# Optimization experiments

Measured on AMD Instinct MI355X. Metric: run time of the kernel, lower is better.

Reference implementation:

```python
import jax, jax.numpy as jnp
import numpy as np
import math

B, T, D_MODEL, N_HEADS = 4, 2048, 1024, 16
HEAD_DIM = D_MODEL // N_HEADS


def setup_inputs() -> dict:
    key = jax.random.key(0)
    k1, k2, k3 = jax.random.split(key, 3)
    x = jax.random.normal(k1, (B, T, D_MODEL), dtype=jnp.float32)
    # torch Linear weight layout: [out_features, in_features]
    w_qkv = jax.random.normal(k2, (3 * D_MODEL, D_MODEL), dtype=jnp.float32) * (1.0 / math.sqrt(D_MODEL))
    w_out = jax.random.normal(k3, (D_MODEL, D_MODEL), dtype=jnp.float32) * (1.0 / math.sqrt(D_MODEL))
    return {"x": x, "w_qkv": w_qkv, "w_out": w_out}


def reference(x, w_qkv, w_out):
    b, t, c = x.shape
    h, d = N_HEADS, HEAD_DIM
    # qkv projection: (B,T,3C) -> (3,B,H,T,D)
    qkv = jnp.einsum('btc,fc->btf', x, w_qkv)
    qkv = qkv.reshape(b, t, 3, h, d).transpose(2, 0, 3, 1, 4)
    q, k, v = qkv[0], qkv[1], qkv[2]
    scale = 1.0 / math.sqrt(d)
    # full O(T^2) attention scores, causal masked
    scores = jnp.einsum('bhqd,bhkd->bhqk', q, k) * scale
    causal = jnp.tril(jnp.ones((t, t), dtype=bool))
    scores = jnp.where(causal[None, None, :, :], scores, jnp.float32(-jnp.inf))
    attn = jax.nn.softmax(scores, axis=-1)
    out = jnp.einsum('bhqk,bhkd->bhqd', attn, v)  # (B,H,T,D)
    out = out.transpose(0, 2, 1, 3).reshape(b, t, c)
    out = jnp.einsum('btc,oc->bto', out, w_out)
    return out
```

## Files before the change

kernel.cpp:

```cpp
#include <hip/hip_runtime.h>
#include <hip/hip_bf16.h>

#define T_SEQ 2048
#define BATCH 4
#define NH    16
#define DM    1024
#define HD    64

typedef __attribute__((ext_vector_type(4))) float  f32x4;
typedef __attribute__((ext_vector_type(8))) short  s16x8;
typedef __attribute__((ext_vector_type(4))) short  s16x4;
typedef __attribute__((ext_vector_type(4))) unsigned short u16x4;

__device__ __forceinline__ unsigned short f2b(float f) {
  union { float f; unsigned u; } v; v.f = f;
  unsigned u = v.u;
  unsigned r = 0x7fffu + ((u >> 16) & 1u);
  u += r;
  return (unsigned short)(u >> 16);
}

__device__ __forceinline__ f32x4 mfma16(s16x8 a, s16x8 b, f32x4 c) {
  return __builtin_amdgcn_mfma_f32_16x16x32_bf16(a, b, c, 0, 0, 0);
}

__global__ void cvt_all(const float* __restrict__ x, const float* __restrict__ wq,
                        const float* __restrict__ wo,
                        unsigned short* __restrict__ xb, unsigned short* __restrict__ wqb,
                        unsigned short* __restrict__ wob) {
  const int N4X = (BATCH * T_SEQ * DM) / 4;
  const int N4Q = (3 * DM * DM) / 4;
  const int N4O = (DM * DM) / 4;
  const int N4QSCALED = (DM * DM) / 4;
  int i = blockIdx.x * blockDim.x + threadIdx.x;
  int stride = gridDim.x * blockDim.x;
  for (int j = i; j < N4X + N4Q + N4O; j += stride) {
    const float* src; unsigned short* dst; int k; float scale = 1.f;
    if (j < N4X) { src = x; dst = xb; k = j; }
    else if (j < N4X + N4Q) {
      k = j - N4X; src = wq; dst = wqb;
      if (k < N4QSCALED) scale = 0.125f;
    } else { k = j - N4X - N4Q; src = wo; dst = wob; }
    f32x4 v = ((const f32x4*)src)[k];
    s16x4 o;
    o.x = (short)f2b(v.x * scale); o.y = (short)f2b(v.y * scale);
    o.z = (short)f2b(v.z * scale); o.w = (short)f2b(v.w * scale);
    ((s16x4*)dst)[k] = o;
  }
}

template<int OUT_F32>
__global__ __launch_bounds__(256)
void gemm_bt(const unsigned short* __restrict__ A,
             const unsigned short* __restrict__ B,
             void* __restrict__ C, int M, int N, int K) {
  __shared__ unsigned short As[128 * 32];
  __shared__ unsigned short Bs[128 * 32];
  const int tid  = threadIdx.x;
  const int lane = tid & 63;
  const int w    = tid >> 6;
  const int wr   = w >> 1, wc = w & 1;
  const int lr   = lane & 15, g = lane >> 4;

  const int gx  = gridDim.x, nwg = gx * gridDim.y;
  const int bid = blockIdx.y * gx + blockIdx.x;
  const int qq  = nwg >> 3;
  const int b2  = (bid & 7) * qq + (bid >> 3);
  const int row0 = (b2 % gx) * 128;
  const int col0 = (b2 / gx) * 128;

  const int srow = w * 16 + (lane >> 2);
  const int scol = (lane & 3) * 8;

  f32x4 acc[4][4] = {};

  for (int kt = 0; kt < K; kt += 32) {
    __syncthreads();
#pragma unroll
    for (int s = 0; s < 2; ++s) {
      const unsigned short* srcA = A + (size_t)(row0 + s * 64 + srow) * K + kt + scol;
      __builtin_amdgcn_global_load_lds((const void*)srcA, (void*)&As[(s * 64 + w * 16) * 32], 16, 0, 0);
      const unsigned short* srcB = B + (size_t)(col0 + s * 64 + srow) * K + kt + scol;
      __builtin_amdgcn_global_load_lds((const void*)srcB, (void*)&Bs[(s * 64 + w * 16) * 32], 16, 0, 0);
    }
    __syncthreads();

    s16x8 af[4], bf[4];
#pragma unroll
    for (int m = 0; m < 4; ++m)
      af[m] = *(const s16x8*)&As[(wr * 64 + m * 16 + lr) * 32 + g * 8];
#pragma unroll
    for (int n = 0; n < 4; ++n)
      bf[n] = *(const s16x8*)&Bs[(wc * 64 + n * 16 + lr) * 32 + g * 8];
#pragma unroll
    for (int m = 0; m < 4; ++m)
#pragma unroll
      for (int n = 0; n < 4; ++n)
        acc[m][n] = mfma16(af[m], bf[n], acc[m][n]);
  }

#pragma unroll
  for (int m = 0; m < 4; ++m)
#pragma unroll
    for (int n = 0; n < 4; ++n)
#pragma unroll
      for (int i = 0; i < 4; ++i) {
        int row = row0 + wr * 64 + m * 16 + g * 4 + i;
        int col = col0 + wc * 64 + n * 16 + lr;
        if (OUT_F32)
          ((float*)C)[(size_t)row * N + col] = acc[m][n][i];
        else
          ((unsigned short*)C)[(size_t)row * N + col] = f2b(acc[m][n][i]);
      }
}

__global__ __launch_bounds__(512)
void attn_kernel(const unsigned short* __restrict__ qkv,
                 unsigned short* __restrict__ out) {
  __shared__ unsigned short Ks[2][64 * 64];
  __shared__ unsigned short Vt[2][64 * 72];
  __shared__ unsigned short Ps[8][16 * 72];

  const int tid  = threadIdx.x;
  const int lane = tid & 63;
  const int w    = tid >> 6;
  const int lr   = lane & 15, g = lane >> 4;
  const int bid  = blockIdx.x;
  const int bh   = bid & 63;
  const int slot = bid >> 6;
  const int qt   = (slot & 1) ? (slot >> 1) : (15 - (slot >> 1));
  const int b    = bh >> 4, h = bh & 15;
  const int q0   = qt * 128;
  const int qr   = q0 + w * 16;
  const int qq   = qr + lr;
  const size_t rb = (size_t)b * T_SEQ;

  s16x8 qf[2];
  {
    const unsigned short* qp = qkv + (rb + qq) * 3072 + h * 64;
    qf[0] = *(const s16x8*)(qp + g * 8);
    qf[1] = *(const s16x8*)(qp + 32 + g * 8);
  }

  float mI = -1e30f, lI = 0.f;
  f32x4 o[4] = {};

  const int nt   = 2 * qt + 2;
  const int qmax = qr + 15;

  const bool grpV = (tid < 256);
  const int vd0 = (tid & 7) * 8, vr0 = (tid >> 3) * 2;
  const int t2  = tid - 256;
  const int kr0 = t2 >> 3, kc0 = t2 & 7;

  s16x8 pre0, pre1;
  {
    if (grpV) {
      const unsigned short* vp = &qkv[(rb + vr0) * 3072 + 2048 + h * 64 + vd0];
      pre0 = *(const s16x8*)vp;
      pre1 = *(const s16x8*)(vp + 3072);
    } else {
      const unsigned short* kp = &qkv[(rb + kr0) * 3072 + 1024 + h * 64 + kc0 * 8];
      pre0 = *(const s16x8*)kp;
      pre1 = *(const s16x8*)(kp + 32 * 3072);
    }
  }

  for (int t = 0; t < nt; ++t) {
    const int cur = t & 1;
    if (grpV) {
#pragma unroll
      for (int jj = 0; jj < 8; ++jj) {
        int d = vd0 + jj;
        int sw = ((d ^ (d >> 3)) & 7) << 4;
        unsigned val = (unsigned)(unsigned short)pre0[jj] |
                       ((unsigned)(unsigned short)pre1[jj] << 16);
        *(unsigned*)((char*)&Vt[cur][0] + d * 144 + ((vr0 * 2) ^ sw)) = val;
      }
    } else {
      *(s16x8*)((char*)&Ks[cur][0] + kr0 * 128 + ((kc0 * 16) ^ ((kr0 & 7) << 4))) = pre0;
      int kr1 = kr0 + 32;
      *(s16x8*)((char*)&Ks[cur][0] + kr1 * 128 + ((kc0 * 16) ^ ((kr1 & 7) << 4))) = pre1;
    }
    __syncthreads();

    if (t + 1 < nt) {
      const int kv0n = (t + 1) * 64;
      if (grpV) {
        const unsigned short* vp = &qkv[(rb + kv0n + vr0) * 3072 + 2048 + h * 64 + vd0];
        pre0 = *(const s16x8*)vp;
        pre1 = *(const s16x8*)(vp + 3072);
      } else {
        const unsigned short* kp = &qkv[(rb + kv0n + kr0) * 3072 + 1024 + h * 64 + kc0 * 8];
        pre0 = *(const s16x8*)kp;
        pre1 = *(const s16x8*)(kp + 32 * 3072);
      }
    }

    const int kv0 = t * 64;
    if (kv0 <= qmax) {
      f32x4 s4[4];
      __builtin_amdgcn_s_setprio(1);
#pragma unroll
      for (int kc = 0; kc < 4; ++kc) {
        int row = kc * 16 + lr;
        const char* kbase = (const char*)&Ks[cur][0] + row * 128;
        int sw = (row & 7) << 4;
        s16x8 kf0 = *(const s16x8*)(kbase + ((g * 16) ^ sw));
        s16x8 kf1 = *(const s16x8*)(kbase + ((64 + g * 16) ^ sw));
        f32x4 s = {};
        s = mfma16(kf0, qf[0], s);
        s = mfma16(kf1, qf[1], s);
        s4[kc] = s;
      }
      __builtin_amdgcn_s_setprio(0);

      if (kv0 + 63 > qr) {
#pragma unroll
        for (int kc = 0; kc < 4; ++kc)
#pragma unroll
          for (int i = 0; i < 4; ++i) {
            int key = kv0 + kc * 16 + g * 4 + i;
            if (key > qq) s4[kc][i] = -1e30f;
          }
      }

      float mx = fmaxf(fmaxf(fmaxf(s4[0][0], s4[0][1]), fmaxf(s4[0][2], s4[0][3])),
                 fmaxf(fmaxf(fmaxf(s4[1][0], s4[1][1]), fmaxf(s4[1][2], s4[1][3])),
                 fmaxf(fmaxf(fmaxf(s4[2][0], s4[2][1]), fmaxf(s4[2][2], s4[2][3])),
                       fmaxf(fmaxf(s4[3][0], s4[3][1]), fmaxf(s4[3][2], s4[3][3])))));
      mx = fmaxf(mx, __shfl_xor(mx, 16));
      mx = fmaxf(mx, __shfl_xor(mx, 32));

      const bool defer = __all(mx - mI <= 8.f);
      float alpha;
      if (defer) {
        alpha = 1.f;
      } else {
        float mn = fmaxf(mI, mx);
        alpha = __expf(mI - mn);
        mI = mn;
      }
      float rs = 0.f;
#pragma unroll
      for (int kc = 0; kc < 4; ++kc)
#pragma unroll
        for (int i = 0; i < 4; ++i) {
          float p = __expf(s4[kc][i] - mI);
          s4[kc][i] = p;
          rs += p;
        }
      rs += __shfl_xor(rs, 16);
      rs += __shfl_xor(rs, 32);
      lI = lI * alpha + rs;

      {
        char* pw = (char*)&Ps[w][0] + lr * 144;
#pragma unroll
        for (int kc = 0; kc < 4; ++kc) {
          unsigned v0 = (unsigned)f2b(s4[kc][0]) | ((unsigned)f2b(s4[kc][1]) << 16);
          unsigned v1 = (unsigned)f2b(s4[kc][2]) | ((unsigned)f2b(s4[kc][3]) << 16);
          unsigned long long pv = (unsigned long long)v0 | ((unsigned long long)v1 << 32);
          *(unsigned long long*)(pw + kc * 32 + g * 8) = pv;
        }
      }

      if (!defer) {
#pragma unroll
        for (int n = 0; n < 4; ++n)
#pragma unroll
          for (int i = 0; i < 4; ++i)
            o[n][i] *= alpha;
      }

      asm volatile("s_waitcnt lgkmcnt(0)" ::: "memory");

      __builtin_amdgcn_s_setprio(1);
#pragma unroll
      for (int kk = 0; kk < 2; ++kk) {
        s16x8 pf = *(const s16x8*)((const char*)&Ps[w][0] + lr * 144 + kk * 64 + g * 16);
#pragma unroll
        for (int n = 0; n < 4; ++n) {
          int d = n * 16 + lr;
          int sw = ((d ^ (d >> 3)) & 7) << 4;
          s16x8 vf = *(const s16x8*)((const char*)&Vt[cur][0] + d * 144 + ((kk * 64 + g * 16) ^ sw));
          o[n] = mfma16(vf, pf, o[n]);
        }
      }
      __builtin_amdgcn_s_setprio(0);
    }
  }

  float rl = 1.f / lI;
#pragma unroll
  for (int n = 0; n < 4; ++n) {
    u16x4 pk;
#pragma unroll
    for (int i = 0; i < 4; ++i) pk[i] = f2b(o[n][i] * rl);
    *(u16x4*)&out[(rb + qq) * 1024 + h * 64 + n * 16 + g * 4] = pk;
  }
}

extern "C" void kernel_launch(void* const* d_in, const int* in_sizes, int n_in,
                              void* d_out, int out_size, void* d_ws, size_t ws_size,
                              hipStream_t stream) {
  const float* x     = (const float*)d_in[0];
  const float* w_qkv = (const float*)d_in[1];
  const float* w_out = (const float*)d_in[2];

  const size_t n_x   = (size_t)BATCH * T_SEQ * DM;
  const size_t n_wq  = (size_t)3 * DM * DM;
  const size_t n_wo  = (size_t)DM * DM;
  const size_t n_qkv = (size_t)BATCH * T_SEQ * 3 * DM;
  const size_t need  = (n_x + n_wq + n_wo + n_qkv + n_x) * 2;
  if (ws_size < need) return;

  unsigned short* xb  = (unsigned short*)d_ws;
  unsigned short* wqb = xb + n_x;
  unsigned short* wob = wqb + n_wq;
  unsigned short* qkv = wob + n_wo;
  unsigned short* att = qkv + n_qkv;

  cvt_all<<<2048, 256, 0, stream>>>(x, w_qkv, w_out, xb, wqb, wob);

  gemm_bt<0><<<dim3(64, 24), 256, 0, stream>>>(xb, wqb, qkv, BATCH * T_SEQ, 3 * DM, DM);
  attn_kernel<<<1024, 512, 0, stream>>>(qkv, att);
  gemm_bt<1><<<dim3(64, 8), 256, 0, stream>>>(att, wob, d_out, BATCH * T_SEQ, DM, DM);
}
```

Measured before the change: 209.3 us.

## Pair causal query tiles per block and use exp2 with hardware bf16 packing

Each attention block now processes two query tiles, qt and 15-qt, in sequence, so every block does the same amount of causal work. The grid is halved to 512 blocks. The softmax scale is folded with log2(e) into the Q weights so the raw v_exp_f32 (exp2) instruction replaces __expf, and the deferred-rescale threshold is adjusted to match the base-2 domain. Manual bf16 rounding is replaced by the v_cvt_pk_bf16_f32 instruction. With fewer blocks, fewer waves are resident to hide latency, and each block's run is serialized over two tiles.

```diff
diff --git a/kernel.cpp b/kernel.cpp
--- a/kernel.cpp
+++ b/kernel.cpp
@@ -22,6 +22,14 @@
 
 __device__ __forceinline__ f32x4 mfma16(s16x8 a, s16x8 b, f32x4 c) {
   return __builtin_amdgcn_mfma_f32_16x16x32_bf16(a, b, c, 0, 0, 0);
+}
+
+__device__ __forceinline__ float exp2_fast(float x) {
+  float r; asm("v_exp_f32 %0, %1" : "=v"(r) : "v"(x)); return r;
+}
+
+__device__ __forceinline__ unsigned cvt_pk_bf16(float lo, float hi) {
+  unsigned r; asm("v_cvt_pk_bf16_f32 %0, %1, %2" : "=v"(r) : "v"(lo), "v"(hi)); return r;
 }
 
 __global__ void cvt_all(const float* __restrict__ x, const float* __restrict__ wq,
@@ -39,7 +47,7 @@
     if (j < N4X) { src = x; dst = xb; k = j; }
     else if (j < N4X + N4Q) {
       k = j - N4X; src = wq; dst = wqb;
-      if (k < N4QSCALED) scale = 0.125f;
+      if (k < N4QSCALED) scale = 0.18033688011112042f;
     } else { k = j - N4X - N4Q; src = wo; dst = wob; }
     f32x4 v = ((const f32x4*)src)[k];
     s16x4 o;
@@ -64,8 +72,8 @@
 
   const int gx  = gridDim.x, nwg = gx * gridDim.y;
   const int bid = blockIdx.y * gx + blockIdx.x;
-  const int qq  = nwg >> 3;
-  const int b2  = (bid & 7) * qq + (bid >> 3);
+  const int cpx = nwg >> 3;
+  const int b2  = (bid & 7) * cpx + (bid >> 3);
   const int row0 = (b2 % gx) * 128;
   const int col0 = (b2 / gx) * 128;
 
@@ -127,177 +135,180 @@
   const int lr   = lane & 15, g = lane >> 4;
   const int bid  = blockIdx.x;
   const int bh   = bid & 63;
-  const int slot = bid >> 6;
-  const int qt   = (slot & 1) ? (slot >> 1) : (15 - (slot >> 1));
+  const int pi   = bid >> 6;
   const int b    = bh >> 4, h = bh & 15;
-  const int q0   = qt * 128;
-  const int qr   = q0 + w * 16;
-  const int qq   = qr + lr;
   const size_t rb = (size_t)b * T_SEQ;
-
-  s16x8 qf[2];
-  {
-    const unsigned short* qp = qkv + (rb + qq) * 3072 + h * 64;
-    qf[0] = *(const s16x8*)(qp + g * 8);
-    qf[1] = *(const s16x8*)(qp + 32 + g * 8);
-  }
-
-  float mI = -1e30f, lI = 0.f;
-  f32x4 o[4] = {};
-
-  const int nt   = 2 * qt + 2;
-  const int qmax = qr + 15;
 
   const bool grpV = (tid < 256);
   const int vd0 = (tid & 7) * 8, vr0 = (tid >> 3) * 2;
   const int t2  = tid - 256;
   const int kr0 = t2 >> 3, kc0 = t2 & 7;
 
-  s16x8 pre0, pre1;
-  {
-    if (grpV) {
-      const unsigned short* vp = &qkv[(rb + vr0) * 3072 + 2048 + h * 64 + vd0];
-      pre0 = *(const s16x8*)vp;
-      pre1 = *(const s16x8*)(vp + 3072);
-    } else {
-      const unsigned short* kp = &qkv[(rb + kr0) * 3072 + 1024 + h * 64 + kc0 * 8];
-      pre0 = *(const s16x8*)kp;
-      pre1 = *(const s16x8*)(kp + 32 * 3072);
-    }
-  }
-
-  for (int t = 0; t < nt; ++t) {
-    const int cur = t & 1;
-    if (grpV) {
-#pragma unroll
-      for (int jj = 0; jj < 8; ++jj) {
-        int d = vd0 + jj;
-        int sw = ((d ^ (d >> 3)) & 7) << 4;
-        unsigned val = (unsigned)(unsigned short)pre0[jj] |
-                       ((unsigned)(unsigned short)pre1[jj] << 16);
-        *(unsigned*)((char*)&Vt[cur][0] + d * 144 + ((vr0 * 2) ^ sw)) = val;
-      }
-    } else {
-      *(s16x8*)((char*)&Ks[cur][0] + kr0 * 128 + ((kc0 * 16) ^ ((kr0 & 7) << 4))) = pre0;
-      int kr1 = kr0 + 32;
-      *(s16x8*)((char*)&Ks[cur][0] + kr1 * 128 + ((kc0 * 16) ^ ((kr1 & 7) << 4))) = pre1;
-    }
-    __syncthreads();
-
-    if (t + 1 < nt) {
-      const int kv0n = (t + 1) * 64;
+#pragma unroll 1
+  for (int ph = 0; ph < 2; ++ph) {
+    const int qt = ph ? (15 - pi) : pi;
+    const int q0 = qt * 128;
+    const int qr = q0 + w * 16;
+    const int qq = qr + lr;
+    const int nt = 2 * qt + 2;
+    const int qmax = qr + 15;
+
+    s16x8 qf[2];
+    {
+      const unsigned short* qp = qkv + (rb + qq) * 3072 + h * 64;
+      qf[0] = *(const s16x8*)(qp + g * 8);
+      qf[1] = *(const s16x8*)(qp + 32 + g * 8);
+    }
+
+    float mI = -1e30f, lI = 0.f;
+    f32x4 o[4] = {};
+
+    s16x8 pre0, pre1;
+    {
       if (grpV) {
-        const unsigned short* vp = &qkv[(rb + kv0n + vr0) * 3072 + 2048 + h * 64 + vd0];
+        const unsigned short* vp = &qkv[(rb + vr0) * 3072 + 2048 + h * 64 + vd0];
         pre0 = *(const s16x8*)vp;
         pre1 = *(const s16x8*)(vp + 3072);
       } else {
-        const unsigned short* kp = &qkv[(rb + kv0n + kr0) * 3072 + 1024 + h * 64 + kc0 * 8];
+        const unsigned short* kp = &qkv[(rb + kr0) * 3072 + 1024 + h * 64 + kc0 * 8];
         pre0 = *(const s16x8*)kp;
         pre1 = *(const s16x8*)(kp + 32 * 3072);
       }
     }
 
-    const int kv0 = t * 64;
-    if (kv0 <= qmax) {
-      f32x4 s4[4];
-      __builtin_amdgcn_s_setprio(1);
-#pragma unroll
-      for (int kc = 0; kc < 4; ++kc) {
-        int row = kc * 16 + lr;
-        const char* kbase = (const char*)&Ks[cur][0] + row * 128;
-        int sw = (row & 7) << 4;
-        s16x8 kf0 = *(const s16x8*)(kbase + ((g * 16) ^ sw));
-        s16x8 kf1 = *(const s16x8*)(kbase + ((64 + g * 16) ^ sw));
-        f32x4 s = {};
-        s = mfma16(kf0, qf[0], s);
-        s = mfma16(kf1, qf[1], s);
-        s4[kc] = s;
-      }
-      __builtin_amdgcn_s_setprio(0);
-
-      if (kv0 + 63 > qr) {
+    for (int t = 0; t < nt; ++t) {
+      const int cur = t & 1;
+      if (grpV) {
+#pragma unroll
+        for (int jj = 0; jj < 8; ++jj) {
+          int d = vd0 + jj;
+          int sw = ((d ^ (d >> 3)) & 7) << 4;
+          unsigned val = (unsigned)(unsigned short)pre0[jj] |
+                         ((unsigned)(unsigned short)pre1[jj] << 16);
+          *(unsigned*)((char*)&Vt[cur][0] + d * 144 + ((vr0 * 2) ^ sw)) = val;
+        }
+      } else {
+        *(s16x8*)((char*)&Ks[cur][0] + kr0 * 128 + ((kc0 * 16) ^ ((kr0 & 7) << 4))) = pre0;
+        int kr1 = kr0 + 32;
+        *(s16x8*)((char*)&Ks[cur][0] + kr1 * 128 + ((kc0 * 16) ^ ((kr1 & 7) << 4))) = pre1;
+      }
+      __syncthreads();
+
+      if (t + 1 < nt) {
+        const int kv0n = (t + 1) * 64;
+        if (grpV) {
+          const unsigned short* vp = &qkv[(rb + kv0n + vr0) * 3072 + 2048 + h * 64 + vd0];
+          pre0 = *(const s16x8*)vp;
+          pre1 = *(const s16x8*)(vp + 3072);
+        } else {
+          const unsigned short* kp = &qkv[(rb + kv0n + kr0) * 3072 + 1024 + h * 64 + kc0 * 8];
+          pre0 = *(const s16x8*)kp;
+          pre1 = *(const s16x8*)(kp + 32 * 3072);
+        }
+      }
+
+      const int kv0 = t * 64;
+      if (kv0 <= qmax) {
+        f32x4 s4[4];
+        __builtin_amdgcn_s_setprio(1);
+#pragma unroll
+        for (int kc = 0; kc < 4; ++kc) {
+          int row = kc * 16 + lr;
+          const char* kbase = (const char*)&Ks[cur][0] + row * 128;
+          int sw = (row & 7) << 4;
+          s16x8 kf0 = *(const s16x8*)(kbase + ((g * 16) ^ sw));
+          s16x8 kf1 = *(const s16x8*)(kbase + ((64 + g * 16) ^ sw));
+          f32x4 s = {};
+          s = mfma16(kf0, qf[0], s);
+          s = mfma16(kf1, qf[1], s);
+          s4[kc] = s;
+        }
+        __builtin_amdgcn_s_setprio(0);
+
+        if (kv0 + 63 > qr) {
+#pragma unroll
+          for (int kc = 0; kc < 4; ++kc)
+#pragma unroll
+            for (int i = 0; i < 4; ++i) {
+              int key = kv0 + kc * 16 + g * 4 + i;
+              if (key > qq) s4[kc][i] = -1e30f;
+            }
+        }
+
+        float mx = fmaxf(fmaxf(fmaxf(s4[0][0], s4[0][1]), fmaxf(s4[0][2], s4[0][3])),
+                   fmaxf(fmaxf(fmaxf(s4[1][0], s4[1][1]), fmaxf(s4[1][2], s4[1][3])),
+                   fmaxf(fmaxf(fmaxf(s4[2][0], s4[2][1]), fmaxf(s4[2][2], s4[2][3])),
+                         fmaxf(fmaxf(s4[3][0], s4[3][1]), fmaxf(s4[3][2], s4[3][3])))));
+        mx = fmaxf(mx, __shfl_xor(mx, 16));
+        mx = fmaxf(mx, __shfl_xor(mx, 32));
+
+        const bool defer = __all(mx - mI <= 11.5f);
+        float alpha;
+        if (defer) {
+          alpha = 1.f;
+        } else {
+          float mn = fmaxf(mI, mx);
+          alpha = exp2_fast(mI - mn);
+          mI = mn;
+        }
+        float rs = 0.f;
 #pragma unroll
         for (int kc = 0; kc < 4; ++kc)
 #pragma unroll
           for (int i = 0; i < 4; ++i) {
-            int key = kv0 + kc * 16 + g * 4 + i;
-            if (key > qq) s4[kc][i] = -1e30f;
+            float p = exp2_fast(s4[kc][i] - mI);
+            s4[kc][i] = p;
+            rs += p;
           }
-      }
-
-      float mx = fmaxf(fmaxf(fmaxf(s4[0][0], s4[0][1]), fmaxf(s4[0][2], s4[0][3])),
-                 fmaxf(fmaxf(fmaxf(s4[1][0], s4[1][1]), fmaxf(s4[1][2], s4[1][3])),
-                 fmaxf(fmaxf(fmaxf(s4[2][0], s4[2][1]), fmaxf(s4[2][2], s4[2][3])),
-                       fmaxf(fmaxf(s4[3][0], s4[3][1]), fmaxf(s4[3][2], s4[3][3])))));
-      mx = fmaxf(mx, __shfl_xor(mx, 16));
-      mx = fmaxf(mx, __shfl_xor(mx, 32));
-
-      const bool defer = __all(mx - mI <= 8.f);
-      float alpha;
-      if (defer) {
-        alpha = 1.f;
-      } else {
-        float mn = fmaxf(mI, mx);
-        alpha = __expf(mI - mn);
-        mI = mn;
-      }
-      float rs = 0.f;
-#pragma unroll
-      for (int kc = 0; kc < 4; ++kc)
-#pragma unroll
-        for (int i = 0; i < 4; ++i) {
-          float p = __expf(s4[kc][i] - mI);
-          s4[kc][i] = p;
-          rs += p;
-        }
-      rs += __shfl_xor(rs, 16);
-      rs += __shfl_xor(rs, 32);
-      lI = lI * alpha + rs;
-
-      {
-        char* pw = (char*)&Ps[w][0] + lr * 144;
-#pragma unroll
-        for (int kc = 0; kc < 4; ++kc) {
-          unsigned v0 = (unsigned)f2b(s4[kc][0]) | ((unsigned)f2b(s4[kc][1]) << 16);
-          unsigned v1 = (unsigned)f2b(s4[kc][2]) | ((unsigned)f2b(s4[kc][3]) << 16);
-          unsigned long long pv = (unsigned long long)v0 | ((unsigned long long)v1 << 32);
-          *(unsigned long long*)(pw + kc * 32 + g * 8) = pv;
-        }
-      }
-
-      if (!defer) {
-#pragma unroll
-        for (int n = 0; n < 4; ++n)
-#pragma unroll
-          for (int i = 0; i < 4; ++i)
-            o[n][i] *= alpha;
-      }
-
-      asm volatile("s_waitcnt lgkmcnt(0)" ::: "memory");
-
-      __builtin_amdgcn_s_setprio(1);
-#pragma unroll
-      for (int kk = 0; kk < 2; ++kk) {
-        s16x8 pf = *(const s16x8*)((const char*)&Ps[w][0] + lr * 144 + kk * 64 + g * 16);
-#pragma unroll
-        for (int n = 0; n < 4; ++n) {
-          int d = n * 16 + lr;
-          int sw = ((d ^ (d >> 3)) & 7) << 4;
-          s16x8 vf = *(const s16x8*)((const char*)&Vt[cur][0] + d * 144 + ((kk * 64 + g * 16) ^ sw));
-          o[n] = mfma16(vf, pf, o[n]);
-        }
-      }
-      __builtin_amdgcn_s_setprio(0);
-    }
-  }
-
-  float rl = 1.f / lI;
-#pragma unroll
-  for (int n = 0; n < 4; ++n) {
-    u16x4 pk;
-#pragma unroll
-    for (int i = 0; i < 4; ++i) pk[i] = f2b(o[n][i] * rl);
-    *(u16x4*)&out[(rb + qq) * 1024 + h * 64 + n * 16 + g * 4] = pk;
+        rs += __shfl_xor(rs, 16);
+        rs += __shfl_xor(rs, 32);
+        lI = lI * alpha + rs;
+
+        {
+          char* pw = (char*)&Ps[w][0] + lr * 144;
+#pragma unroll
+          for (int kc = 0; kc < 4; ++kc) {
+            unsigned v0 = cvt_pk_bf16(s4[kc][0], s4[kc][1]);
+            unsigned v1 = cvt_pk_bf16(s4[kc][2], s4[kc][3]);
+            unsigned long long pv = (unsigned long long)v0 | ((unsigned long long)v1 << 32);
+            *(unsigned long long*)(pw + kc * 32 + g * 8) = pv;
+          }
+        }
+
+        if (!defer) {
+#pragma unroll
+          for (int n = 0; n < 4; ++n)
+#pragma unroll
+            for (int i = 0; i < 4; ++i)
+              o[n][i] *= alpha;
+        }
+
+        asm volatile("s_waitcnt lgkmcnt(0)" ::: "memory");
+
+        __builtin_amdgcn_s_setprio(1);
+#pragma unroll
+        for (int kk = 0; kk < 2; ++kk) {
+          s16x8 pf = *(const s16x8*)((const char*)&Ps[w][0] + lr * 144 + kk * 64 + g * 16);
+#pragma unroll
+          for (int n = 0; n < 4; ++n) {
+            int d = n * 16 + lr;
+            int sw = ((d ^ (d >> 3)) & 7) << 4;
+            s16x8 vf = *(const s16x8*)((const char*)&Vt[cur][0] + d * 144 + ((kk * 64 + g * 16) ^ sw));
+            o[n] = mfma16(vf, pf, o[n]);
+          }
+        }
+        __builtin_amdgcn_s_setprio(0);
+      }
+    }
+
+    float rl = 1.f / lI;
+#pragma unroll
+    for (int n = 0; n < 4; ++n) {
+      unsigned p0 = cvt_pk_bf16(o[n][0] * rl, o[n][1] * rl);
+      unsigned p1 = cvt_pk_bf16(o[n][2] * rl, o[n][3] * rl);
+      unsigned long long pv = (unsigned long long)p0 | ((unsigned long long)p1 << 32);
+      *(unsigned long long*)&out[(rb + qq) * 1024 + h * 64 + n * 16 + g * 4] = pv;
+    }
   }
 }
 
@@ -324,6 +335,6 @@
   cvt_all<<<2048, 256, 0, stream>>>(x, w_qkv, w_out, xb, wqb, wob);
 
   gemm_bt<0><<<dim3(64, 24), 256, 0, stream>>>(xb, wqb, qkv, BATCH * T_SEQ, 3 * DM, DM);
-  attn_kernel<<<1024, 512, 0, stream>>>(qkv, att);
+  attn_kernel<<<512, 512, 0, stream>>>(qkv, att);
   gemm_bt<1><<<dim3(64, 8), 256, 0, stream>>>(att, wob, d_out, BATCH * T_SEQ, DM, DM);
 }
```

Result: faster. 200.2 us (-4.3%).
